# Performance work log

Measured on AMD Instinct MI355X. Metric: run time of the kernel, lower is better.

## Reference

```python
import jax, jax.numpy as jnp
import numpy as np

N_NODES = 100000
HIDDEN = 128
N_LAYERS = 3
N_EDGES = 600000


def setup_inputs() -> dict:
    key = jax.random.key(0)
    k_e, k_emb, k_w = jax.random.split(key, 3)
    edge_index = jax.random.randint(k_e, (2, N_EDGES), 0, N_NODES, dtype=jnp.int64 if jax.config.read('jax_enable_x64') else jnp.int32)
    embedding = jax.random.normal(k_emb, (N_NODES, HIDDEN), dtype=jnp.float32)
    Ws = jax.random.normal(k_w, (N_LAYERS, HIDDEN, HIDDEN), dtype=jnp.float32) * (1.0 / np.sqrt(HIDDEN))
    bs = jnp.zeros((N_LAYERS, HIDDEN), dtype=jnp.float32)
    return {"edge_index": edge_index, "embedding": embedding, "Ws": Ws, "bs": bs}


def _gcn_forward(embedding, Ws, bs, edge_index):
    N = embedding.shape[0]
    # PyG GCNConv default: add self-loops, symmetric deg^{-1/2} normalization
    loop = jnp.arange(N, dtype=edge_index.dtype)
    src = jnp.concatenate([edge_index[0], loop])  # [E+N]
    dst = jnp.concatenate([edge_index[1], loop])
    deg = jax.ops.segment_sum(jnp.ones_like(dst, dtype=embedding.dtype), dst, num_segments=N)
    dinv = jnp.where(deg > 0, jax.lax.rsqrt(jnp.where(deg > 0, deg, 1.0)), 0.0)
    norm = dinv[src] * dinv[dst]  # [E+N]

    x = embedding
    for l in range(Ws.shape[0]):
        h = x @ Ws[l]                              # [N, d] linear transform
        msg = h[src] * norm[:, None]               # gather + scale
        x = jax.ops.segment_sum(msg, dst, num_segments=N) + bs[l]  # scatter-add
        x = jax.nn.relu(x)
        # dropout is identity in eval mode
    return x


def reference(edge_index, embedding, Ws, bs):
    return _gcn_forward(embedding, Ws, bs, edge_index)
```

## Files before the change

kernel.cpp:

```cpp
#include <hip/hip_runtime.h>
#include <hip/hip_bf16.h>


#define HID 128

typedef __attribute__((ext_vector_type(8))) short short8;
typedef __attribute__((ext_vector_type(4))) float floatx4;

#define WLDS 136


__global__ void k_init_cnt(int* cnt, int n) {
    int i = blockIdx.x * blockDim.x + threadIdx.x;
    if (i < n) cnt[i] = 1;
}

__global__ void k_count_edges(const int* __restrict__ ei, int* cnt, int E) {
    int e = blockIdx.x * blockDim.x + threadIdx.x;
    if (e < E) atomicAdd(&cnt[ei[E + e]], 1);
}

__global__ void k_scanA(const int* __restrict__ cnt, int* csum, int n) {
    __shared__ int sd[256];
    int t = threadIdx.x;
    int base = blockIdx.x * 1024 + t * 4;
    int s = 0;
#pragma unroll
    for (int j = 0; j < 4; j++) { int i = base + j; if (i < n) s += cnt[i]; }
    sd[t] = s; __syncthreads();
    for (int off = 128; off > 0; off >>= 1) {
        if (t < off) sd[t] += sd[t + off];
        __syncthreads();
    }
    if (t == 0) csum[blockIdx.x] = sd[0];
}

__global__ void k_scanB(int* csum, int* offsets, int nchunk, int n) {
    __shared__ int sd[256];
    int t = threadIdx.x;
    int v = (t < nchunk) ? csum[t] : 0;
    sd[t] = v; __syncthreads();
    for (int off = 1; off < 256; off <<= 1) {
        int u = (t >= off) ? sd[t - off] : 0;
        __syncthreads();
        sd[t] += u;
        __syncthreads();
    }
    if (t < nchunk) csum[t] = sd[t] - v;
    if (t == 0) offsets[n] = sd[255];
}

__global__ void k_scanC(const int* __restrict__ cnt, const int* __restrict__ csum,
                        int* offsets, int* cursor, float* dinv,
                        int* adj_src, float* adj_norm, int n) {
    __shared__ int sd[256];
    int t = threadIdx.x;
    int base = blockIdx.x * 1024 + t * 4;
    int c[4]; int s = 0;
#pragma unroll
    for (int j = 0; j < 4; j++) {
        c[j] = (base + j < n) ? cnt[base + j] : 0;
        s += c[j];
    }
    sd[t] = s; __syncthreads();
    for (int off = 1; off < 256; off <<= 1) {
        int v = (t >= off) ? sd[t - off] : 0;
        __syncthreads();
        sd[t] += v;
        __syncthreads();
    }
    int run = sd[t] - s + csum[blockIdx.x];
#pragma unroll
    for (int j = 0; j < 4; j++) {
        int i = base + j;
        if (i < n) {
            offsets[i] = run;
            float di = rsqrtf((float)c[j]);
            dinv[i] = di;
            cursor[i] = run + 1;
            adj_src[run] = i;
            adj_norm[run] = di * di;
        }
        run += c[j];
    }
}

__global__ void k_fill_edges(const int* __restrict__ ei, int* cursor,
                             const float* __restrict__ dinv,
                             int* adj_src, float* adj_norm, int E) {
    int e = blockIdx.x * blockDim.x + threadIdx.x;
    if (e >= E) return;
    int s = ei[e];
    int d = ei[E + e];
    int pos = atomicAdd(&cursor[d], 1);
    adj_src[pos] = s;
    adj_norm[pos] = dinv[s] * dinv[d];
}

__global__ void k_packW(const float* __restrict__ Ws, ushort* Whp, ushort* Wlp,
                        int nlayers) {
    int idx = blockIdx.x * blockDim.x + threadIdx.x;
    if (idx >= nlayers * HID * HID) return;
    int l = idx >> 14;
    int n = (idx >> 7) & 127;
    int k = idx & 127;
    float w = Ws[(size_t)l * HID * HID + k * HID + n];
    __hip_bfloat16 hi = __float2bfloat16(w);
    float lo = w - __bfloat162float(hi);
    __hip_bfloat16 lo16 = __float2bfloat16(lo);
    Whp[idx] = *(ushort*)&hi;
    Wlp[idx] = *(ushort*)&lo16;
}


__global__ __launch_bounds__(256) void k_agg(const float* __restrict__ x,
                                             const int* __restrict__ offsets,
                                             const int* __restrict__ adj_src,
                                             const float* __restrict__ adj_norm,
                                             ushort* __restrict__ yh,
                                             ushort* __restrict__ yl, int n) {
    int gid = blockIdx.x * blockDim.x + threadIdx.x;
    int node = gid >> 6;
    int lane = gid & 63;
    if (node >= n) return;
    int beg = offsets[node];
    int end = offsets[node + 1];
    int q    = lane >> 4;
    int ql   = lane & 15;
    int f4   = (q & 1) * 16 + ql;
    int epar = q >> 1;
    float4 acc = {0.f, 0.f, 0.f, 0.f};
#pragma unroll 2
    for (int e = beg; e < end; e += 2) {
        int me = e + epar;
        int mc = me < end ? me : end - 1;
        int s  = adj_src[mc];
        float w = me < end ? adj_norm[mc] : 0.f;
        float4 v = ((const float4*)(x + (size_t)s * HID))[f4];
        acc.x += w * v.x;
        acc.y += w * v.y;
        acc.z += w * v.z;
        acc.w += w * v.w;
    }
    acc.x += __shfl_xor(acc.x, 32);
    acc.y += __shfl_xor(acc.y, 32);
    acc.z += __shfl_xor(acc.z, 32);
    acc.w += __shfl_xor(acc.w, 32);
    if (lane < 32) {
        float a[4] = {acc.x, acc.y, acc.z, acc.w};
        ushort4 h, l;
        ushort* hp = (ushort*)&h;
        ushort* lp = (ushort*)&l;
#pragma unroll
        for (int j = 0; j < 4; j++) {
            __hip_bfloat16 hi = __float2bfloat16(a[j]);
            float lo = a[j] - __bfloat162float(hi);
            __hip_bfloat16 lo16 = __float2bfloat16(lo);
            hp[j] = *(ushort*)&hi;
            lp[j] = *(ushort*)&lo16;
        }
        ((ushort4*)(yh + (size_t)node * HID))[lane] = h;
        ((ushort4*)(yl + (size_t)node * HID))[lane] = l;
    }
}


__global__ __launch_bounds__(256, 2) void k_gemm_mfma(const ushort* __restrict__ yh,
                                                      const ushort* __restrict__ yl,
                                                      const ushort* __restrict__ Whp,
                                                      const ushort* __restrict__ Wlp,
                                                      const float* __restrict__ bias,
                                                      float* __restrict__ out, int n) {
    __shared__ ushort Wh_lds[HID * WLDS];
    __shared__ ushort Wl_lds[HID * WLDS];
    int t = threadIdx.x;
    int wave = t >> 6;
    int lane = t & 63;
    int m16  = lane & 15;
    int oct  = lane >> 4;

    short8 ah[2][4], al[2][4];
#pragma unroll
    for (int mt = 0; mt < 2; mt++) {
        int rowA = blockIdx.x * 128 + wave * 32 + mt * 16 + m16;
        const ushort* hb = yh + (size_t)rowA * HID + oct * 8;
        const ushort* lb = yl + (size_t)rowA * HID + oct * 8;
#pragma unroll
        for (int ks = 0; ks < 4; ks++) {
            ah[mt][ks] = *(const short8*)(hb + ks * 32);
            al[mt][ks] = *(const short8*)(lb + ks * 32);
        }
    }

    for (int idx = t; idx < HID * 16; idx += 256) {
        int r = idx >> 4, c8 = idx & 15;
        ((uint4*)(Wh_lds + r * WLDS))[c8] = ((const uint4*)(Whp + r * HID))[c8];
        ((uint4*)(Wl_lds + r * WLDS))[c8] = ((const uint4*)(Wlp + r * HID))[c8];
    }
    __syncthreads();

    floatx4 acc0[8], acc1[8];
#pragma unroll
    for (int c = 0; c < 8; c++) {
        acc0[c] = (floatx4){0.f, 0.f, 0.f, 0.f};
        acc1[c] = (floatx4){0.f, 0.f, 0.f, 0.f};
    }

#pragma unroll
    for (int ks = 0; ks < 4; ks++) {
#pragma unroll
        for (int c = 0; c < 8; c++) {
            const ushort* bp = Wh_lds + (c * 16 + m16) * WLDS + ks * 32 + oct * 8;
            const ushort* bq = Wl_lds + (c * 16 + m16) * WLDS + ks * 32 + oct * 8;
            short8 bh = *(const short8*)bp;
            short8 bl = *(const short8*)bq;
            acc0[c] = __builtin_amdgcn_mfma_f32_16x16x32_bf16(ah[0][ks], bh, acc0[c], 0, 0, 0);
            acc0[c] = __builtin_amdgcn_mfma_f32_16x16x32_bf16(ah[0][ks], bl, acc0[c], 0, 0, 0);
            acc0[c] = __builtin_amdgcn_mfma_f32_16x16x32_bf16(al[0][ks], bh, acc0[c], 0, 0, 0);
            acc1[c] = __builtin_amdgcn_mfma_f32_16x16x32_bf16(ah[1][ks], bh, acc1[c], 0, 0, 0);
            acc1[c] = __builtin_amdgcn_mfma_f32_16x16x32_bf16(ah[1][ks], bl, acc1[c], 0, 0, 0);
            acc1[c] = __builtin_amdgcn_mfma_f32_16x16x32_bf16(al[1][ks], bh, acc1[c], 0, 0, 0);
        }
    }

#pragma unroll
    for (int mt = 0; mt < 2; mt++) {
        int rowbase = blockIdx.x * 128 + wave * 32 + mt * 16 + oct * 4;
#pragma unroll
        for (int c = 0; c < 8; c++) {
            int col = c * 16 + m16;
            float b = bias[col];
            floatx4 a = mt == 0 ? acc0[c] : acc1[c];
#pragma unroll
            for (int r = 0; r < 4; r++) {
                int row = rowbase + r;
                if (row < n) {
                    float v = fmaxf(a[r] + b, 0.f);
                    out[(size_t)row * HID + col] = v;
                }
            }
        }
    }
}


extern "C" void kernel_launch(void* const* d_in, const int* in_sizes, int n_in,
                              void* d_out, int out_size, void* d_ws, size_t ws_size,
                              hipStream_t stream) {
    const int* ei = (const int*)d_in[0];
    const float* emb = (const float*)d_in[1];
    const float* Ws = (const float*)d_in[2];
    const float* bs = (const float*)d_in[3];

    const int E = in_sizes[0] / 2;
    const int N = in_sizes[1] / HID;
    const int NL = in_sizes[3] / HID;
    const int TOT = E + N;
    const int NPAD = ((N + 127) / 128) * 128;

    char* p = (char*)d_ws;
    auto carve = [&](size_t bytes) {
        char* r = p;
        p += (bytes + 255) & ~(size_t)255;
        return (void*)r;
    };
    int*    cnt      = (int*)   carve((size_t)N * 4);
    int*    offsets  = (int*)   carve((size_t)(N + 1) * 4);
    int*    cursor   = (int*)   carve((size_t)N * 4);
    float*  dinv     = (float*) carve((size_t)N * 4);
    int*    csum     = (int*)   carve(1024 * 4);
    int*    adj_src  = (int*)   carve((size_t)TOT * 4);
    float*  adj_norm = (float*) carve((size_t)TOT * 4);
    ushort* yh       = (ushort*)carve((size_t)NPAD * HID * 2);
    ushort* yl       = (ushort*)carve((size_t)NPAD * HID * 2);
    ushort* Whp      = (ushort*)carve((size_t)NL * HID * HID * 2);
    ushort* Wlp      = (ushort*)carve((size_t)NL * HID * HID * 2);
    float*  xbufA    = (float*) carve((size_t)N * HID * 4);
    float*  xbufB    = (float*) d_out;

    const int NCHUNK = (N + 1023) / 1024;

    k_init_cnt<<<(N + 255) / 256, 256, 0, stream>>>(cnt, N);
    k_count_edges<<<(E + 255) / 256, 256, 0, stream>>>(ei, cnt, E);
    k_scanA<<<NCHUNK, 256, 0, stream>>>(cnt, csum, N);
    k_scanB<<<1, 256, 0, stream>>>(csum, offsets, NCHUNK, N);
    k_scanC<<<NCHUNK, 256, 0, stream>>>(cnt, csum, offsets, cursor, dinv,
                                        adj_src, adj_norm, N);
    k_fill_edges<<<(E + 255) / 256, 256, 0, stream>>>(ei, cursor, dinv,
                                                      adj_src, adj_norm, E);
    k_packW<<<(NL * HID * HID + 255) / 256, 256, 0, stream>>>(Ws, Whp, Wlp, NL);

    const int aggBlocks = (N * 64 + 255) / 256;
    const int gemmBlocks = NPAD / 128;
    const float* x = emb;
    for (int l = 0; l < NL; l++) {
        float* o = (l == 1) ? xbufA : xbufB;
        k_agg<<<aggBlocks, 256, 0, stream>>>(x, offsets, adj_src, adj_norm, yh, yl, N);
        k_gemm_mfma<<<gemmBlocks, 256, 0, stream>>>(yh, yl,
                                                    Whp + (size_t)l * HID * HID,
                                                    Wlp + (size_t)l * HID * HID,
                                                    bs + (size_t)l * HID, o, N);
        x = o;
    }
}
```

Baseline: 439.2 us.

## Use a persistent grid-stride wave loop and software-pipeline neighbor gathers in aggregation

The aggregation kernel now launches a fixed grid of 2048 blocks, and each wave loops over nodes in grid-stride fashion instead of one wave per node. Inside the edge loop, the index/weight loads are prefetched two steps ahead and the feature row load one step ahead, so gather latency overlaps with the FMAs. This aims to hide the latency of the dependent index-then-row memory accesses and cut block launch overhead. In exchange it raises register pressure, and load balance across waves may suffer when node degrees vary.

```diff
diff --git a/kernel.cpp b/kernel.cpp
--- a/kernel.cpp
+++ b/kernel.cpp
@@ -120,47 +120,72 @@
                                              ushort* __restrict__ yh,
                                              ushort* __restrict__ yl, int n) {
     int gid = blockIdx.x * blockDim.x + threadIdx.x;
-    int node = gid >> 6;
     int lane = gid & 63;
-    if (node >= n) return;
-    int beg = offsets[node];
-    int end = offsets[node + 1];
     int q    = lane >> 4;
     int ql   = lane & 15;
     int f4   = (q & 1) * 16 + ql;
     int epar = q >> 1;
-    float4 acc = {0.f, 0.f, 0.f, 0.f};
-#pragma unroll 2
-    for (int e = beg; e < end; e += 2) {
-        int me = e + epar;
-        int mc = me < end ? me : end - 1;
-        int s  = adj_src[mc];
-        float w = me < end ? adj_norm[mc] : 0.f;
-        float4 v = ((const float4*)(x + (size_t)s * HID))[f4];
-        acc.x += w * v.x;
-        acc.y += w * v.y;
-        acc.z += w * v.z;
-        acc.w += w * v.w;
-    }
-    acc.x += __shfl_xor(acc.x, 32);
-    acc.y += __shfl_xor(acc.y, 32);
-    acc.z += __shfl_xor(acc.z, 32);
-    acc.w += __shfl_xor(acc.w, 32);
-    if (lane < 32) {
-        float a[4] = {acc.x, acc.y, acc.z, acc.w};
-        ushort4 h, l;
-        ushort* hp = (ushort*)&h;
-        ushort* lp = (ushort*)&l;
-#pragma unroll
-        for (int j = 0; j < 4; j++) {
-            __hip_bfloat16 hi = __float2bfloat16(a[j]);
-            float lo = a[j] - __bfloat162float(hi);
-            __hip_bfloat16 lo16 = __float2bfloat16(lo);
-            hp[j] = *(ushort*)&hi;
-            lp[j] = *(ushort*)&lo16;
-        }
-        ((ushort4*)(yh + (size_t)node * HID))[lane] = h;
-        ((ushort4*)(yl + (size_t)node * HID))[lane] = l;
+    int nwaves = (gridDim.x * blockDim.x) >> 6;
+
+    for (int node = gid >> 6; node < n; node += nwaves) {
+        int beg = offsets[node];
+        int end = offsets[node + 1];
+
+        float4 acc = {0.f, 0.f, 0.f, 0.f};
+
+        int e0 = beg + epar;
+        int c0 = e0 < end ? e0 : end - 1;
+        int s0 = adj_src[c0];
+        float w0 = e0 < end ? adj_norm[c0] : 0.f;
+
+        int e1 = beg + 2 + epar;
+        int c1 = e1 < end ? e1 : end - 1;
+        int s1 = adj_src[c1];
+        float w1 = e1 < end ? adj_norm[c1] : 0.f;
+
+        float4 v0 = ((const float4*)(x + (size_t)s0 * HID))[f4];
+
+        for (int e = beg + 2; e < end; e += 2) {
+            int e2 = e + 2 + epar;
+            int c2 = e2 < end ? e2 : end - 1;
+            int s2 = adj_src[c2];
+            float w2 = e2 < end ? adj_norm[c2] : 0.f;
+
+            float4 v1 = ((const float4*)(x + (size_t)s1 * HID))[f4];
+
+            acc.x += w0 * v0.x;
+            acc.y += w0 * v0.y;
+            acc.z += w0 * v0.z;
+            acc.w += w0 * v0.w;
+
+            v0 = v1; w0 = w1;
+            s1 = s2; w1 = w2;
+        }
+        acc.x += w0 * v0.x;
+        acc.y += w0 * v0.y;
+        acc.z += w0 * v0.z;
+        acc.w += w0 * v0.w;
+
+        acc.x += __shfl_xor(acc.x, 32);
+        acc.y += __shfl_xor(acc.y, 32);
+        acc.z += __shfl_xor(acc.z, 32);
+        acc.w += __shfl_xor(acc.w, 32);
+        if (lane < 32) {
+            float a[4] = {acc.x, acc.y, acc.z, acc.w};
+            ushort4 h, l;
+            ushort* hp = (ushort*)&h;
+            ushort* lp = (ushort*)&l;
+#pragma unroll
+            for (int j = 0; j < 4; j++) {
+                __hip_bfloat16 hi = __float2bfloat16(a[j]);
+                float lo = a[j] - __bfloat162float(hi);
+                __hip_bfloat16 lo16 = __float2bfloat16(lo);
+                hp[j] = *(ushort*)&hi;
+                lp[j] = *(ushort*)&lo16;
+            }
+            ((ushort4*)(yh + (size_t)node * HID))[lane] = h;
+            ((ushort4*)(yl + (size_t)node * HID))[lane] = l;
+        }
     }
 }
 
@@ -290,7 +315,7 @@
                                                       adj_src, adj_norm, E);
     k_packW<<<(NL * HID * HID + 255) / 256, 256, 0, stream>>>(Ws, Whp, Wlp, NL);
 
-    const int aggBlocks = (N * 64 + 255) / 256;
+    const int aggBlocks = 2048;
     const int gemmBlocks = NPAD / 128;
     const float* x = emb;
     for (int l = 0; l < NL; l++) {
```

Measured after the change: 430.2 us. 2.0% less time.
